# Optimization experiments

Hardware: AMD Instinct MI355X
Metric: run time of the kernel (lower is better)

## Reference

```python
import jax, jax.numpy as jnp
import numpy as np
from jax import lax

BIG = 1.0e6  # sentinel distance when a row contains no foreground pixel


def _dist1d(fg):
    """Exact 1D distance (in pixels) to nearest True along the last axis.

    fg: bool [..., W]. Returns float32 [..., W]; BIG where no True in the row.
    """
    W = fg.shape[-1]
    idx = jnp.arange(W, dtype=jnp.int32)
    # nearest foreground index to the left (inclusive)
    last = lax.cummax(jnp.where(fg, idx, -1), axis=fg.ndim - 1)
    d_left = jnp.where(last >= 0, (idx - last).astype(jnp.float32), BIG)
    # nearest foreground to the right: same scan on the reversed row
    fr = fg[..., ::-1]
    lastr = lax.cummax(jnp.where(fr, idx, -1), axis=fg.ndim - 1)
    d_right = jnp.where(lastr >= 0, (idx - lastr).astype(jnp.float32), BIG)[..., ::-1]
    return jnp.minimum(d_left, d_right)


def _edt2d(gt):
    """Exact Euclidean distance transform: distance from each pixel to the
    nearest gt==1 pixel (== scipy.distance_transform_edt(1-gt)).

    gt: [B, H, W] int. Returns float32 [B, H, W].
    Separable decomposition: D2(i,w) = min_j (d_row(j,w)^2 + (i-j)^2).
    """
    H = gt.shape[1]
    d_row = _dist1d(gt > 0)            # [B, H, W] 1D distances along rows
    dr2 = d_row * d_row                # squared row distances
    i = jnp.arange(H, dtype=jnp.float32)
    offs = (i[:, None] - i[None, :]) ** 2            # [Hi, Hj]
    # [B, Hi, Hj, W] = dr2 broadcast over i  +  (i-j)^2 broadcast over b, w
    d2 = jnp.min(dr2[:, None, :, :] + offs[None, :, :, None], axis=2)
    return jnp.sqrt(d2)


def setup_inputs() -> dict:
    key = jax.random.key(0)
    k1, k2 = jax.random.split(key)
    B, C, H, W = 8, 1, 256, 256
    logits = jax.random.normal(k1, (B, C, H, W), dtype=jnp.float32)
    target = jax.random.randint(k2, (B, C, H, W), 0, 2, dtype=jnp.int32)
    return {"logits": logits, "target": target}


def reference(logits, target):
    prob = jax.nn.sigmoid(logits)                      # [B, 1, H, W]
    D_gt = _edt2d(target[:, 0, :, :])[:, None, :, :]   # [B, 1, H, W]
    return jnp.mean(prob * D_gt)
```

## Files before the change

kernel.cpp:

```cpp
#include <hip/hip_runtime.h>


#define BIGF 1000000.0f
#define BIG2 (BIGF * BIGF)

constexpr int B = 8;
constexpr int H = 256;
constexpr int W = 256;
constexpr int NPIX = B * H * W;

__device__ __forceinline__ float block_reduce_sum_256(float v) {
    #pragma unroll
    for (int off = 32; off > 0; off >>= 1)
        v += __shfl_down(v, off, 64);
    __shared__ float s[4];
    const int lane = threadIdx.x & 63;
    const int wid  = threadIdx.x >> 6;
    if (lane == 0) s[wid] = v;
    __syncthreads();
    if (wid == 0) {
        v = (lane < 4) ? s[lane] : 0.0f;
        v += __shfl_down(v, 2, 64);
        v += __shfl_down(v, 1, 64);
    }
    return v;
}

__device__ __forceinline__ void upd16(const float4 m, float j0,
                                      float n0, float n1, float n2, float n3,
                                      float& b0, float& b1, float& b2, float& b3) {
    const float j1 = j0 + 1.0f, j2 = j0 + 2.0f, j3 = j0 + 3.0f;
    {
        const float c0 = fmaf(n0, j0, m.x), c1 = fmaf(n0, j1, m.y);
        const float c2 = fmaf(n0, j2, m.z), c3 = fmaf(n0, j3, m.w);
        b0 = fminf(b0, fminf(fminf(c0, c1), fminf(c2, c3)));
    }
    {
        const float c0 = fmaf(n1, j0, m.x), c1 = fmaf(n1, j1, m.y);
        const float c2 = fmaf(n1, j2, m.z), c3 = fmaf(n1, j3, m.w);
        b1 = fminf(b1, fminf(fminf(c0, c1), fminf(c2, c3)));
    }
    {
        const float c0 = fmaf(n2, j0, m.x), c1 = fmaf(n2, j1, m.y);
        const float c2 = fmaf(n2, j2, m.z), c3 = fmaf(n2, j3, m.w);
        b2 = fminf(b2, fminf(fminf(c0, c1), fminf(c2, c3)));
    }
    {
        const float c0 = fmaf(n3, j0, m.x), c1 = fmaf(n3, j1, m.y);
        const float c2 = fmaf(n3, j2, m.z), c3 = fmaf(n3, j3, m.w);
        b3 = fminf(b3, fminf(fminf(c0, c1), fminf(c2, c3)));
    }
}

__global__ __launch_bounds__(256) void row_dist_kernel(
        const int* __restrict__ target, float* __restrict__ dr2) {
    __shared__ float s_q[4][256];
    const int lane = threadIdx.x & 63;
    const int wv   = threadIdx.x >> 6;
    const int row  = (blockIdx.x << 2) + wv;

    const int4 tv = *(const int4*)(target + row * W + (lane << 2));
    const float fj0 = (float)(lane << 2);
    const float fj1 = fj0 + 1.0f, fj2 = fj0 + 2.0f, fj3 = fj0 + 3.0f;
    float4 q;
    q.x = fmaf(fj0, fj0, tv.x > 0 ? 0.0f : BIG2);
    q.y = fmaf(fj1, fj1, tv.y > 0 ? 0.0f : BIG2);
    q.z = fmaf(fj2, fj2, tv.z > 0 ? 0.0f : BIG2);
    q.w = fmaf(fj3, fj3, tv.w > 0 ? 0.0f : BIG2);
    *(float4*)&s_q[wv][lane << 2] = q;
    __syncthreads();

    const float w0f = (float)lane,         w1f = (float)(lane + 64);
    const float w2f = (float)(lane + 128), w3f = (float)(lane + 192);
    const float n0 = -2.0f * w0f, n1 = -2.0f * w1f;
    const float n2 = -2.0f * w2f, n3 = -2.0f * w3f;
    float b0 = 4e12f, b1 = 4e12f, b2 = 4e12f, b3 = 4e12f;

    float fj = 0.0f;
    #pragma unroll 4
    for (int jv = 0; jv < 64; ++jv, fj += 4.0f) {
        const float4 m = *(const float4*)&s_q[wv][jv << 2];
        upd16(m, fj, n0, n1, n2, n3, b0, b1, b2, b3);
    }

    const int base = row * W + lane;
    dr2[base]       = fmaf(w0f, w0f, b0);
    dr2[base + 64]  = fmaf(w1f, w1f, b1);
    dr2[base + 128] = fmaf(w2f, w2f, b2);
    dr2[base + 192] = fmaf(w3f, w3f, b3);
}

__global__ __launch_bounds__(256) void col_pass_kernel(
        const float* __restrict__ logits, const float* __restrict__ dr2,
        float* __restrict__ partials) {
    __shared__ float s_q[4][256];
    const int t  = threadIdx.x;
    const int b  = blockIdx.x >> 6;
    const int w0 = (blockIdx.x & 63) << 2;

    const float4 v  = *(const float4*)(dr2 + (b * H + t) * W + w0);
    const float fj  = (float)t;
    const float fj2 = fj * fj;
    s_q[0][t] = fj2 + v.x;
    s_q[1][t] = fj2 + v.y;
    s_q[2][t] = fj2 + v.z;
    s_q[3][t] = fj2 + v.w;
    __syncthreads();

    const int lane = t & 63;
    const int wv   = t >> 6;
    const float i0f = (float)lane,         i1f = (float)(lane + 64);
    const float i2f = (float)(lane + 128), i3f = (float)(lane + 192);
    const float n0 = -2.0f * i0f, n1 = -2.0f * i1f;
    const float n2 = -2.0f * i2f, n3 = -2.0f * i3f;
    float b0 = 4e12f, b1 = 4e12f, b2 = 4e12f, b3 = 4e12f;

    float fjv = 0.0f;
    #pragma unroll 4
    for (int jv = 0; jv < 64; ++jv, fjv += 4.0f) {
        const float4 m = *(const float4*)&s_q[wv][jv << 2];
        upd16(m, fjv, n0, n1, n2, n3, b0, b1, b2, b3);
    }

    const int wcol = w0 + wv;
    const int base = (b * H + lane) * W + wcol;
    float acc;
    {
        const float dist = sqrtf(fmaf(i0f, i0f, b0));
        const float x = logits[base];
        acc = dist / (1.0f + expf(-x));
    }
    {
        const float dist = sqrtf(fmaf(i1f, i1f, b1));
        const float x = logits[base + 64 * W];
        acc += dist / (1.0f + expf(-x));
    }
    {
        const float dist = sqrtf(fmaf(i2f, i2f, b2));
        const float x = logits[base + 128 * W];
        acc += dist / (1.0f + expf(-x));
    }
    {
        const float dist = sqrtf(fmaf(i3f, i3f, b3));
        const float x = logits[base + 192 * W];
        acc += dist / (1.0f + expf(-x));
    }

    const float s = block_reduce_sum_256(acc);
    if (t == 0) partials[blockIdx.x] = s;
}

__global__ __launch_bounds__(256) void final_reduce_kernel(
        const float* __restrict__ partials, float* __restrict__ out,
        int n, float scale) {
    float v = 0.0f;
    for (int idx = threadIdx.x; idx < n; idx += 256)
        v += partials[idx];
    v = block_reduce_sum_256(v);
    if (threadIdx.x == 0) out[0] = v * scale;
}

extern "C" void kernel_launch(void* const* d_in, const int* in_sizes, int n_in,
                              void* d_out, int out_size, void* d_ws, size_t ws_size,
                              hipStream_t stream) {
    const float* logits = (const float*)d_in[0];
    const int*   target = (const int*)d_in[1];

    float* dr2      = (float*)d_ws;
    float* partials = dr2 + NPIX;

    row_dist_kernel<<<B * H / 4, 256, 0, stream>>>(target, dr2);
    col_pass_kernel<<<B * W / 4, 256, 0, stream>>>(logits, dr2, partials);
    final_reduce_kernel<<<1, 256, 0, stream>>>(partials, (float*)d_out,
                                               B * W / 4, 1.0f / (float)NPIX);
}
```

Measured before the change: 74.68 us.

## Replace brute-force row min with wave scans and fuse final reduction

The row pass no longer does an O(W^2) brute-force min over squared distances. It now finds the nearest foreground pixel to the left and right with wave-level shuffle prefix max/min scans, which is linear work per row. The separate final reduction kernel is removed: the last col-pass block, detected through an atomic counter that the row kernel resets, sums the partials. This saves a launch, but the design depends on the counter reset being ordered before the col kernel runs and on a correct threadfence pattern.

```diff
diff --git a/kernel.cpp b/kernel.cpp
--- a/kernel.cpp
+++ b/kernel.cpp
@@ -3,6 +3,7 @@
 
 #define BIGF 1000000.0f
 #define BIG2 (BIGF * BIGF)
+#define BIGI (1 << 20)
 
 constexpr int B = 8;
 constexpr int H = 256;
@@ -53,46 +54,78 @@
 }
 
 __global__ __launch_bounds__(256) void row_dist_kernel(
-        const int* __restrict__ target, float* __restrict__ dr2) {
-    __shared__ float s_q[4][256];
+        const int* __restrict__ target, float* __restrict__ dr2,
+        unsigned* __restrict__ counter) {
     const int lane = threadIdx.x & 63;
     const int wv   = threadIdx.x >> 6;
     const int row  = (blockIdx.x << 2) + wv;
 
+    if (blockIdx.x == 0 && threadIdx.x == 0) *counter = 0u;
+
     const int4 tv = *(const int4*)(target + row * W + (lane << 2));
-    const float fj0 = (float)(lane << 2);
-    const float fj1 = fj0 + 1.0f, fj2 = fj0 + 2.0f, fj3 = fj0 + 3.0f;
-    float4 q;
-    q.x = fmaf(fj0, fj0, tv.x > 0 ? 0.0f : BIG2);
-    q.y = fmaf(fj1, fj1, tv.y > 0 ? 0.0f : BIG2);
-    q.z = fmaf(fj2, fj2, tv.z > 0 ? 0.0f : BIG2);
-    q.w = fmaf(fj3, fj3, tv.w > 0 ? 0.0f : BIG2);
-    *(float4*)&s_q[wv][lane << 2] = q;
-    __syncthreads();
-
-    const float w0f = (float)lane,         w1f = (float)(lane + 64);
-    const float w2f = (float)(lane + 128), w3f = (float)(lane + 192);
-    const float n0 = -2.0f * w0f, n1 = -2.0f * w1f;
-    const float n2 = -2.0f * w2f, n3 = -2.0f * w3f;
-    float b0 = 4e12f, b1 = 4e12f, b2 = 4e12f, b3 = 4e12f;
-
-    float fj = 0.0f;
-    #pragma unroll 4
-    for (int jv = 0; jv < 64; ++jv, fj += 4.0f) {
-        const float4 m = *(const float4*)&s_q[wv][jv << 2];
-        upd16(m, fj, n0, n1, n2, n3, b0, b1, b2, b3);
-    }
-
-    const int base = row * W + lane;
-    dr2[base]       = fmaf(w0f, w0f, b0);
-    dr2[base + 64]  = fmaf(w1f, w1f, b1);
-    dr2[base + 128] = fmaf(w2f, w2f, b2);
-    dr2[base + 192] = fmaf(w3f, w3f, b3);
+    const int i0 = lane << 2;
+
+    int lastL = -1;
+    if (tv.x > 0) lastL = i0;
+    if (tv.y > 0) lastL = i0 + 1;
+    if (tv.z > 0) lastL = i0 + 2;
+    if (tv.w > 0) lastL = i0 + 3;
+    int incl = lastL;
+    #pragma unroll
+    for (int off = 1; off < 64; off <<= 1) {
+        const int t = __shfl_up(incl, off, 64);
+        if (lane >= off) incl = max(incl, t);
+    }
+    int runL = __shfl_up(incl, 1, 64);
+    if (lane == 0) runL = -1;
+
+    if (tv.x > 0) runL = i0;
+    const int dl0 = (runL >= 0) ? (i0     - runL) : BIGI;
+    if (tv.y > 0) runL = i0 + 1;
+    const int dl1 = (runL >= 0) ? (i0 + 1 - runL) : BIGI;
+    if (tv.z > 0) runL = i0 + 2;
+    const int dl2 = (runL >= 0) ? (i0 + 2 - runL) : BIGI;
+    if (tv.w > 0) runL = i0 + 3;
+    const int dl3 = (runL >= 0) ? (i0 + 3 - runL) : BIGI;
+
+    int nextR = BIGI;
+    if (tv.w > 0) nextR = i0 + 3;
+    if (tv.z > 0) nextR = i0 + 2;
+    if (tv.y > 0) nextR = i0 + 1;
+    if (tv.x > 0) nextR = i0;
+    int inclR = nextR;
+    #pragma unroll
+    for (int off = 1; off < 64; off <<= 1) {
+        const int t = __shfl_down(inclR, off, 64);
+        if (lane < 64 - off) inclR = min(inclR, t);
+    }
+    int runR = __shfl_down(inclR, 1, 64);
+    if (lane == 63) runR = BIGI;
+
+    if (tv.w > 0) runR = i0 + 3;
+    const int dR3 = runR - (i0 + 3);
+    if (tv.z > 0) runR = i0 + 2;
+    const int dR2v = runR - (i0 + 2);
+    if (tv.y > 0) runR = i0 + 1;
+    const int dR1 = runR - (i0 + 1);
+    if (tv.x > 0) runR = i0;
+    const int dR0 = runR - i0;
+
+    const int d0 = min(dl0, dR0), d1 = min(dl1, dR1);
+    const int d2 = min(dl2, dR2v), d3 = min(dl3, dR3);
+    const float f0 = (float)d0, f1 = (float)d1, f2 = (float)d2, f3 = (float)d3;
+    float4 o;
+    o.x = (d0 > 255) ? BIG2 : f0 * f0;
+    o.y = (d1 > 255) ? BIG2 : f1 * f1;
+    o.z = (d2 > 255) ? BIG2 : f2 * f2;
+    o.w = (d3 > 255) ? BIG2 : f3 * f3;
+    *(float4*)(dr2 + row * W + (lane << 2)) = o;
 }
 
 __global__ __launch_bounds__(256) void col_pass_kernel(
         const float* __restrict__ logits, const float* __restrict__ dr2,
-        float* __restrict__ partials) {
+        float* __restrict__ partials, unsigned* __restrict__ counter,
+        float* __restrict__ out) {
     __shared__ float s_q[4][256];
     const int t  = threadIdx.x;
     const int b  = blockIdx.x >> 6;
@@ -147,17 +180,25 @@
     }
 
     const float s = block_reduce_sum_256(acc);
-    if (t == 0) partials[blockIdx.x] = s;
-}
-
-__global__ __launch_bounds__(256) void final_reduce_kernel(
-        const float* __restrict__ partials, float* __restrict__ out,
-        int n, float scale) {
-    float v = 0.0f;
-    for (int idx = threadIdx.x; idx < n; idx += 256)
-        v += partials[idx];
-    v = block_reduce_sum_256(v);
-    if (threadIdx.x == 0) out[0] = v * scale;
+
+    __shared__ bool amLast;
+    if (t == 0) {
+        partials[blockIdx.x] = s;
+        __threadfence();
+        const unsigned prev = atomicAdd(counter, 1u);
+        amLast = (prev == gridDim.x - 1);
+    }
+    __syncthreads();
+    if (amLast) {
+        __threadfence();
+        float fv = __hip_atomic_load(&partials[t], __ATOMIC_RELAXED,
+                                     __HIP_MEMORY_SCOPE_AGENT);
+        fv += __hip_atomic_load(&partials[t + 256], __ATOMIC_RELAXED,
+                                __HIP_MEMORY_SCOPE_AGENT);
+        __syncthreads();
+        const float tot = block_reduce_sum_256(fv);
+        if (t == 0) out[0] = tot * (1.0f / (float)NPIX);
+    }
 }
 
 extern "C" void kernel_launch(void* const* d_in, const int* in_sizes, int n_in,
@@ -166,11 +207,11 @@
     const float* logits = (const float*)d_in[0];
     const int*   target = (const int*)d_in[1];
 
-    float* dr2      = (float*)d_ws;
-    float* partials = dr2 + NPIX;
-
-    row_dist_kernel<<<B * H / 4, 256, 0, stream>>>(target, dr2);
-    col_pass_kernel<<<B * W / 4, 256, 0, stream>>>(logits, dr2, partials);
-    final_reduce_kernel<<<1, 256, 0, stream>>>(partials, (float*)d_out,
-                                               B * W / 4, 1.0f / (float)NPIX);
-}
+    float*    dr2      = (float*)d_ws;
+    float*    partials = dr2 + NPIX;
+    unsigned* counter  = (unsigned*)(partials + 512);
+
+    row_dist_kernel<<<B * H / 4, 256, 0, stream>>>(target, dr2, counter);
+    col_pass_kernel<<<B * W / 4, 256, 0, stream>>>(logits, dr2, partials,
+                                                   counter, (float*)d_out);
+}
```

Result: slower. 80.66 us (+8.0%).

## Fuse row distance pass into column pass using per-thread bitmask row scan

Applied to the files above, without the earlier changes.

Removes the separate brute-force row distance kernel and its intermediate buffer. Each thread in the column kernel now packs its whole target row into 64-bit masks and finds the nearest foreground left and right with clz/ffs, computing exact 1D distances for its four columns. This removes one launch and the dr2 round trip and replaces O(W^2) row work with a bit scan. The cost is that every block rereads full target rows, about 64x redundant target traffic, plus extra register pressure.

```diff
diff --git a/kernel.cpp b/kernel.cpp
--- a/kernel.cpp
+++ b/kernel.cpp
@@ -3,6 +3,7 @@
 
 #define BIGF 1000000.0f
 #define BIG2 (BIGF * BIGF)
+#define BIGI (1 << 20)
 
 constexpr int B = 8;
 constexpr int H = 256;
@@ -52,59 +53,83 @@
     }
 }
 
-__global__ __launch_bounds__(256) void row_dist_kernel(
-        const int* __restrict__ target, float* __restrict__ dr2) {
-    __shared__ float s_q[4][256];
-    const int lane = threadIdx.x & 63;
-    const int wv   = threadIdx.x >> 6;
-    const int row  = (blockIdx.x << 2) + wv;
-
-    const int4 tv = *(const int4*)(target + row * W + (lane << 2));
-    const float fj0 = (float)(lane << 2);
-    const float fj1 = fj0 + 1.0f, fj2 = fj0 + 2.0f, fj3 = fj0 + 3.0f;
-    float4 q;
-    q.x = fmaf(fj0, fj0, tv.x > 0 ? 0.0f : BIG2);
-    q.y = fmaf(fj1, fj1, tv.y > 0 ? 0.0f : BIG2);
-    q.z = fmaf(fj2, fj2, tv.z > 0 ? 0.0f : BIG2);
-    q.w = fmaf(fj3, fj3, tv.w > 0 ? 0.0f : BIG2);
-    *(float4*)&s_q[wv][lane << 2] = q;
-    __syncthreads();
-
-    const float w0f = (float)lane,         w1f = (float)(lane + 64);
-    const float w2f = (float)(lane + 128), w3f = (float)(lane + 192);
-    const float n0 = -2.0f * w0f, n1 = -2.0f * w1f;
-    const float n2 = -2.0f * w2f, n3 = -2.0f * w3f;
-    float b0 = 4e12f, b1 = 4e12f, b2 = 4e12f, b3 = 4e12f;
-
-    float fj = 0.0f;
-    #pragma unroll 4
-    for (int jv = 0; jv < 64; ++jv, fj += 4.0f) {
-        const float4 m = *(const float4*)&s_q[wv][jv << 2];
-        upd16(m, fj, n0, n1, n2, n3, b0, b1, b2, b3);
-    }
-
-    const int base = row * W + lane;
-    dr2[base]       = fmaf(w0f, w0f, b0);
-    dr2[base + 64]  = fmaf(w1f, w1f, b1);
-    dr2[base + 128] = fmaf(w2f, w2f, b2);
-    dr2[base + 192] = fmaf(w3f, w3f, b3);
-}
-
-__global__ __launch_bounds__(256) void col_pass_kernel(
-        const float* __restrict__ logits, const float* __restrict__ dr2,
+__global__ __launch_bounds__(256) void fused_pass_kernel(
+        const float* __restrict__ logits, const int* __restrict__ target,
         float* __restrict__ partials) {
     __shared__ float s_q[4][256];
     const int t  = threadIdx.x;
     const int b  = blockIdx.x >> 6;
     const int w0 = (blockIdx.x & 63) << 2;
 
-    const float4 v  = *(const float4*)(dr2 + (b * H + t) * W + w0);
-    const float fj  = (float)t;
-    const float fj2 = fj * fj;
-    s_q[0][t] = fj2 + v.x;
-    s_q[1][t] = fj2 + v.y;
-    s_q[2][t] = fj2 + v.z;
-    s_q[3][t] = fj2 + v.w;
+    {
+        const int* rowp = target + (b * H + t) * W;
+        unsigned long long wb[4];
+        #pragma unroll
+        for (int g = 0; g < 4; ++g) {
+            unsigned long long acc = 0ull;
+            #pragma unroll
+            for (int k = 0; k < 16; ++k) {
+                const int4 tv = *(const int4*)(rowp + (((g << 4) + k) << 2));
+                unsigned long long nib =
+                    (tv.x > 0 ? 1ull : 0ull) | (tv.y > 0 ? 2ull : 0ull) |
+                    (tv.z > 0 ? 4ull : 0ull) | (tv.w > 0 ? 8ull : 0ull);
+                acc |= nib << (k << 2);
+            }
+            wb[g] = acc;
+        }
+
+        const int kw     = w0 >> 6;
+        const int bshift = w0 & 63;
+        const unsigned long long mlo = (2ull << bshift) - 1ull;
+        const unsigned long long mhi = (~0ull) << (bshift + 3);
+
+        int L = -BIGI;
+        #pragma unroll
+        for (int k = 0; k < 4; ++k) {
+            const unsigned long long vl =
+                (k < kw) ? wb[k] : ((k == kw) ? (wb[k] & mlo) : 0ull);
+            const int candL = (k << 6) + 63 - __clzll((long long)vl);
+            L = vl ? candL : L;
+        }
+        int R3 = BIGI;
+        #pragma unroll
+        for (int k = 3; k >= 0; --k) {
+            const unsigned long long vr =
+                (k > kw) ? wb[k] : ((k == kw) ? (wb[k] & mhi) : 0ull);
+            const int candR = (k << 6) + __ffsll((unsigned long long)vr) - 1;
+            R3 = vr ? candR : R3;
+        }
+
+        const unsigned long long wkw =
+            (kw & 2) ? ((kw & 1) ? wb[3] : wb[2]) : ((kw & 1) ? wb[1] : wb[0]);
+        const unsigned bit0 = (unsigned)(wkw >> bshift)       & 1u;
+        const unsigned bit1 = (unsigned)(wkw >> (bshift + 1)) & 1u;
+        const unsigned bit2 = (unsigned)(wkw >> (bshift + 2)) & 1u;
+        const unsigned bit3 = (unsigned)(wkw >> (bshift + 3)) & 1u;
+
+        const int L0 = L;
+        const int L1 = bit1 ? (w0 + 1) : L0;
+        const int L2 = bit2 ? (w0 + 2) : L1;
+        const int L3 = bit3 ? (w0 + 3) : L2;
+        const int R3c = R3;
+        const int R2 = bit2 ? (w0 + 2) : R3c;
+        const int R1 = bit1 ? (w0 + 1) : R2;
+        const int R0 = bit0 ? (w0 + 0) : R1;
+
+        const int d0 = min(w0     - L0, R0 - w0);
+        const int d1 = min(w0 + 1 - L1, R1 - (w0 + 1));
+        const int d2 = min(w0 + 2 - L2, R2 - (w0 + 2));
+        const int d3 = min(w0 + 3 - L3, R3c - (w0 + 3));
+
+        const float fj  = (float)t;
+        const float fj2 = fj * fj;
+        const float f0 = (float)d0, f1 = (float)d1;
+        const float f2 = (float)d2, f3 = (float)d3;
+        s_q[0][t] = fj2 + ((d0 > 255) ? BIG2 : f0 * f0);
+        s_q[1][t] = fj2 + ((d1 > 255) ? BIG2 : f1 * f1);
+        s_q[2][t] = fj2 + ((d2 > 255) ? BIG2 : f2 * f2);
+        s_q[3][t] = fj2 + ((d3 > 255) ? BIG2 : f3 * f3);
+    }
     __syncthreads();
 
     const int lane = t & 63;
@@ -166,11 +191,9 @@
     const float* logits = (const float*)d_in[0];
     const int*   target = (const int*)d_in[1];
 
-    float* dr2      = (float*)d_ws;
-    float* partials = dr2 + NPIX;
+    float* partials = (float*)d_ws;
 
-    row_dist_kernel<<<B * H / 4, 256, 0, stream>>>(target, dr2);
-    col_pass_kernel<<<B * W / 4, 256, 0, stream>>>(logits, dr2, partials);
+    fused_pass_kernel<<<B * W / 4, 256, 0, stream>>>(logits, target, partials);
     final_reduce_kernel<<<1, 256, 0, stream>>>(partials, (float*)d_out,
                                                B * W / 4, 1.0f / (float)NPIX);
 }
```

Measured after the change: 81.90 us. 9.7% more time.
